# Optimization experiments

Hardware: AMD Instinct MI355X
Metric: run time of the kernel (lower is better)

Reference implementation:

```python
import jax, jax.numpy as jnp
import numpy as np

KERNEL_MUL = 2.0
KERNEL_NUM = 5
EPS = 1e-6


def setup_inputs() -> dict:
    key = jax.random.key(0)
    k1, k2 = jax.random.split(key)
    source = jax.random.normal(k1, (65536, 512), dtype=jnp.float32)
    target = jax.random.normal(k2, (65536, 512), dtype=jnp.float32)
    return {"source": source, "target": target}


def reference(source, target):
    m = source.shape[0]
    m2 = m // 2
    # odd/even index pairing (static shapes)
    x_odd = source[0:m:2][:m2]   # [m2, d]
    x_even = source[1:m:2][:m2]
    y_odd = target[0:m:2][:m2]
    y_even = target[1:m:2][:m2]

    # per-pair squared L2 distances, [m2]
    dxx = jnp.sum((x_odd - x_even) ** 2, axis=-1)
    dyy = jnp.sum((y_odd - y_even) ** 2, axis=-1)
    dxy = jnp.sum((x_odd - y_even) ** 2, axis=-1)
    dyx = jnp.sum((x_even - y_odd) ** 2, axis=-1)

    # per-pair base bandwidth, then multi-bandwidth list [K, m2]
    bw = (dxx + dyy + dxy + dyx) / 4.0
    bw = bw / (KERNEL_MUL ** (KERNEL_NUM // 2))
    mults = KERNEL_MUL ** jnp.arange(KERNEL_NUM, dtype=source.dtype)  # [K]
    bws = bw[None, :] * mults[:, None] + EPS  # [K, m2]

    h = (jnp.exp(-dxx[None, :] / bws)
         + jnp.exp(-dyy[None, :] / bws)
         - jnp.exp(-dxy[None, :] / bws)
         - jnp.exp(-dyx[None, :] / bws)).sum(axis=0)  # [m2]
    return h.mean()
```

## Files before the change

### kernel.cpp

```cpp
#include <hip/hip_runtime.h>


#define D        512
#define M2       32768
#define NBLOCKS  2048
#define NTHREADS 256
#define WAVES_PB (NTHREADS / 64)

__global__ __launch_bounds__(NTHREADS) void mmd_pairs(const float* __restrict__ src,
                                                      const float* __restrict__ tgt,
                                                      float* __restrict__ partial) {
    const int lane = threadIdx.x & 63;
    const int wid  = threadIdx.x >> 6;
    const int stride = NBLOCKS * WAVES_PB;

    float acc = 0.0f;

    for (int pair = blockIdx.x * WAVES_PB + wid; pair < M2; pair += stride) {
        const float* xo = src + (size_t)2 * D * (size_t)pair;
        const float* xe = xo + D;
        const float* yo = tgt + (size_t)2 * D * (size_t)pair;
        const float* ye = yo + D;

        float sxx = 0.f, syy = 0.f, sxy = 0.f, syx = 0.f;

#pragma unroll
        for (int c = 0; c < 2; ++c) {
            const int idx = c * 256 + lane * 4;
            const float4 a  = *reinterpret_cast<const float4*>(xo + idx);
            const float4 b  = *reinterpret_cast<const float4*>(xe + idx);
            const float4 g  = *reinterpret_cast<const float4*>(yo + idx);
            const float4 h4 = *reinterpret_cast<const float4*>(ye + idx);
#define COMP(f)                                   \
            { float t;                            \
              t = a.f - b.f;   sxx += t * t;      \
              t = g.f - h4.f;  syy += t * t;      \
              t = a.f - h4.f;  sxy += t * t;      \
              t = b.f - g.f;   syx += t * t; }
            COMP(x) COMP(y) COMP(z) COMP(w)
#undef COMP
        }

#pragma unroll
        for (int off = 32; off > 0; off >>= 1) {
            sxx += __shfl_xor(sxx, off, 64);
            syy += __shfl_xor(syy, off, 64);
            sxy += __shfl_xor(sxy, off, 64);
            syx += __shfl_xor(syx, off, 64);
        }

        if (lane == 0) {
            const float bw = (sxx + syy + sxy + syx) * 0.25f * 0.25f;
            float h = 0.0f;
            float mult = 1.0f;
#pragma unroll
            for (int k = 0; k < 5; ++k) {
                const float bws = bw * mult + 1e-6f;
                h += expf(-sxx / bws) + expf(-syy / bws)
                   - expf(-sxy / bws) - expf(-syx / bws);
                mult *= 2.0f;
            }
            acc += h;
        }
    }

    __shared__ float red[WAVES_PB];
    if (lane == 0) red[wid] = acc;
    __syncthreads();
    if (threadIdx.x == 0) {
        float s = 0.f;
#pragma unroll
        for (int i = 0; i < WAVES_PB; ++i) s += red[i];
        partial[blockIdx.x] = s;
    }
}

__global__ __launch_bounds__(256) void mmd_final(const float* __restrict__ partial,
                                                 float* __restrict__ out) {
    float s = 0.f;
    for (int i = threadIdx.x; i < NBLOCKS; i += 256) s += partial[i];
#pragma unroll
    for (int off = 32; off > 0; off >>= 1) s += __shfl_xor(s, off, 64);
    __shared__ float red[4];
    if ((threadIdx.x & 63) == 0) red[threadIdx.x >> 6] = s;
    __syncthreads();
    if (threadIdx.x == 0)
        out[0] = (red[0] + red[1] + red[2] + red[3]) * (1.0f / (float)M2);
}

extern "C" void kernel_launch(void* const* d_in, const int* in_sizes, int n_in,
                              void* d_out, int out_size, void* d_ws, size_t ws_size,
                              hipStream_t stream) {
    const float* src = (const float*)d_in[0];
    const float* tgt = (const float*)d_in[1];
    float* out = (float*)d_out;
    float* partial = (float*)d_ws;

    mmd_pairs<<<NBLOCKS, NTHREADS, 0, stream>>>(src, tgt, partial);
    mmd_final<<<1, 256, 0, stream>>>(partial, out);
}
```

Before: 279.2 us.

## Spread exp terms across lanes, unroll pair loop, replace final kernel with atomics

Each pair's 20 exp terms (5 bandwidths x 4 distances) now go to different lanes of the wave instead of being computed serially by lane 0, so every lane accumulates a signed term. The pair loop gets a fixed trip count and is unrolled by 2 so more loads can be in flight. The second reduction kernel is dropped in favour of a memset plus one atomicAdd per block. This makes the float summation order nondeterministic and adds one memset launch.

```diff
diff --git a/kernel.cpp b/kernel.cpp
--- a/kernel.cpp
+++ b/kernel.cpp
@@ -5,21 +5,30 @@
 #define M2       32768
 #define NBLOCKS  2048
 #define NTHREADS 256
-#define WAVES_PB (NTHREADS / 64)
+#define WPB      (NTHREADS / 64)
+#define NWAVES   (NBLOCKS * WPB)
+#define PPW      (M2 / NWAVES)
 
 __global__ __launch_bounds__(NTHREADS) void mmd_pairs(const float* __restrict__ src,
                                                       const float* __restrict__ tgt,
-                                                      float* __restrict__ partial) {
+                                                      float* __restrict__ out) {
     const int lane = threadIdx.x & 63;
     const int wid  = threadIdx.x >> 6;
-    const int stride = NBLOCKS * WAVES_PB;
+    const int wave = blockIdx.x * WPB + wid;
+
+    const int   r    = lane & 3;
+    const int   k    = lane >> 2;
+    const float mult = (float)(1 << k);
+    const float sgn  = (k < 5) ? ((r < 2) ? 1.0f : -1.0f) : 0.0f;
 
     float acc = 0.0f;
 
-    for (int pair = blockIdx.x * WAVES_PB + wid; pair < M2; pair += stride) {
-        const float* xo = src + (size_t)2 * D * (size_t)pair;
+#pragma unroll 2
+    for (int i = 0; i < PPW; ++i) {
+        const int pair = wave + i * NWAVES;
+        const float* xo = src + (size_t)(2 * D) * (size_t)pair;
         const float* xe = xo + D;
-        const float* yo = tgt + (size_t)2 * D * (size_t)pair;
+        const float* yo = tgt + (size_t)(2 * D) * (size_t)pair;
         const float* ye = yo + D;
 
         float sxx = 0.f, syy = 0.f, sxy = 0.f, syx = 0.f;
@@ -49,43 +58,25 @@
             syx += __shfl_xor(syx, off, 64);
         }
 
-        if (lane == 0) {
-            const float bw = (sxx + syy + sxy + syx) * 0.25f * 0.25f;
-            float h = 0.0f;
-            float mult = 1.0f;
-#pragma unroll
-            for (int k = 0; k < 5; ++k) {
-                const float bws = bw * mult + 1e-6f;
-                h += expf(-sxx / bws) + expf(-syy / bws)
-                   - expf(-sxy / bws) - expf(-syx / bws);
-                mult *= 2.0f;
-            }
-            acc += h;
-        }
+        const float bw   = (sxx + syy + sxy + syx) * 0.0625f;
+        const float bws  = bw * mult + 1e-6f;
+        const float dsel = (r & 2) ? ((r & 1) ? syx : sxy)
+                                   : ((r & 1) ? syy : sxx);
+        acc += sgn * expf(-dsel / bws);
     }
 
-    __shared__ float red[WAVES_PB];
+#pragma unroll
+    for (int off = 32; off > 0; off >>= 1) acc += __shfl_xor(acc, off, 64);
+
+    __shared__ float red[WPB];
     if (lane == 0) red[wid] = acc;
     __syncthreads();
     if (threadIdx.x == 0) {
         float s = 0.f;
 #pragma unroll
-        for (int i = 0; i < WAVES_PB; ++i) s += red[i];
-        partial[blockIdx.x] = s;
+        for (int i = 0; i < WPB; ++i) s += red[i];
+        atomicAdd(out, s * (1.0f / (float)M2));
     }
-}
-
-__global__ __launch_bounds__(256) void mmd_final(const float* __restrict__ partial,
-                                                 float* __restrict__ out) {
-    float s = 0.f;
-    for (int i = threadIdx.x; i < NBLOCKS; i += 256) s += partial[i];
-#pragma unroll
-    for (int off = 32; off > 0; off >>= 1) s += __shfl_xor(s, off, 64);
-    __shared__ float red[4];
-    if ((threadIdx.x & 63) == 0) red[threadIdx.x >> 6] = s;
-    __syncthreads();
-    if (threadIdx.x == 0)
-        out[0] = (red[0] + red[1] + red[2] + red[3]) * (1.0f / (float)M2);
 }
 
 extern "C" void kernel_launch(void* const* d_in, const int* in_sizes, int n_in,
@@ -94,8 +85,7 @@
     const float* src = (const float*)d_in[0];
     const float* tgt = (const float*)d_in[1];
     float* out = (float*)d_out;
-    float* partial = (float*)d_ws;
 
-    mmd_pairs<<<NBLOCKS, NTHREADS, 0, stream>>>(src, tgt, partial);
-    mmd_final<<<1, 256, 0, stream>>>(partial, out);
+    hipMemsetAsync(out, 0, sizeof(float), stream);
+    mmd_pairs<<<NBLOCKS, NTHREADS, 0, stream>>>(src, tgt, out);
 }
```

Result: faster. 272.2 us (-2.5%).
